# Optimization experiments

Measured on AMD Instinct MI355X. Metric: run time of the kernel, lower is better.

Reference implementation:

```python
import jax, jax.numpy as jnp
import numpy as np

D_MODEL = 512
N_HEADS = 8
POI_N, POI_F = 1683, 24


def _linear_params(k, fan_in, fan_out):
    kw, kb = jax.random.split(k)
    bound = 1.0 / np.sqrt(fan_in)
    w = jax.random.uniform(kw, (fan_in, fan_out), jnp.float32, -bound, bound)
    b = jax.random.uniform(kb, (fan_out,), jnp.float32, -bound, bound)
    return w, b


def setup_inputs() -> dict:
    key = jax.random.key(0)
    ks = jax.random.split(key, 7)
    B, L, D = 8, 8192, D_MODEL
    x = jax.random.normal(ks[0], (B, L, D), jnp.float32)
    poi_data = jax.random.normal(ks[1], (POI_N, POI_F), jnp.float32)
    wq1, bq1 = _linear_params(ks[2], POI_F, 1)
    wq2, bq2 = _linear_params(ks[3], POI_N, D)
    wk, bk = _linear_params(ks[4], D, D)
    wv, bv = _linear_params(ks[5], D, D)
    wo, bo = _linear_params(ks[6], D, D)
    return dict(x=x, poi_data=poi_data, wq1=wq1, bq1=bq1, wq2=wq2, bq2=bq2,
                wk=wk, bk=bk, wv=wv, bv=bv, wo=wo, bo=bo)


def reference(x, poi_data, wq1, bq1, wq2, bq2, wk, bk, wv, bv, wo, bo):
    B, L, D = x.shape
    H = N_HEADS
    d = D // H
    # key / value projections: [B, L, H, d]
    k = (x @ wk + bk).reshape(B, L, H, d)
    v = (x @ wv + bv).reshape(B, L, H, d)
    # query: Linear(24,1) over poi features, squeeze, Linear(1683, d_model)
    q = (poi_data @ wq1 + bq1)[:, 0]          # [1683]
    q = (q @ wq2 + bq2).reshape(H, d)         # [H, d] -- shared across B and L
    scale = 1.0 / jnp.sqrt(jnp.asarray(d, x.dtype))
    # Original computes scores [B,H,L,L] where every row l is identical
    # (query is broadcast over L). Mathematically equivalent collapsed form:
    scores = jnp.einsum('he,bshe->bhs', q, k)  # [B, H, L]
    A = jax.nn.softmax(scale * scores, axis=-1)
    V = jnp.einsum('bhs,bshd->bhd', A, v).reshape(B, H * d)  # [B, D]
    out = jnp.broadcast_to(V[:, None, :], (B, L, H * d))      # same row for all L
    return out @ wo + bo
```

## Files before the change

kernel.cpp:

```cpp
#include <hip/hip_runtime.h>
#include <math.h>

#define L_SEQ 8192
#define B_N   8

typedef float f4v __attribute__((ext_vector_type(4)));

#define QRAW_OFF   0
#define QF_OFF     2048
#define QKV_OFF    2560
#define CK_OFF     6656
#define V_OFF      6720
#define ROW_OFF    10816
#define DPART_OFF  15360
#define YPART_OFF  32768

__global__ void k01_init(float* ws, const float* __restrict__ poi,
                         const float* __restrict__ wq1, const float* __restrict__ bq1,
                         const float* __restrict__ bv, const float* __restrict__ bo,
                         const float* __restrict__ bq2) {
    int gid = blockIdx.x * 256 + threadIdx.x;
    if (gid < 1683) {
        float a = bq1[0];
#pragma unroll
        for (int j = 0; j < 24; ++j) a += poi[gid * 24 + j] * wq1[j];
        ws[QRAW_OFF + gid] = a;
    } else if (gid >= 2048 && gid < 6144) {
        int i = gid - 2048;
        ws[V_OFF + i] = bv[i & 511];
    } else if (gid >= 6144 && gid < 10240) {
        int i = gid - 6144;
        ws[ROW_OFF + i] = bo[i & 511];
    } else if (gid >= 10240 && gid < 10752) {
        ws[QF_OFF + (gid - 10240)] = bq2[gid - 10240];
    }
}

__global__ __launch_bounds__(512) void k2_qf(const float* __restrict__ wq2, float* ws) {
    __shared__ float qr[32];
    int k = blockIdx.x, t = threadIdx.x;
    int i0 = k * 32;
    int cnt = 1683 - i0; if (cnt > 32) cnt = 32;
    if (t < cnt) qr[t] = ws[QRAW_OFF + i0 + t];
    __syncthreads();
    float a = 0.f;
    for (int ii = 0; ii < cnt; ++ii) a += qr[ii] * wq2[(size_t)(i0 + ii) * 512 + t];
    atomicAdd(ws + QF_OFF + t, a);
}

__global__ void k3_qkvec(const float* __restrict__ wk, const float* __restrict__ bk, float* ws) {
    __shared__ float qf[512];
    int t = threadIdx.x;
    for (int t2 = t; t2 < 512; t2 += 256) qf[t2] = ws[QF_OFF + t2];
    __syncthreads();
    int idx = blockIdx.x * 256 + t;
    int h = idx >> 9, c = idx & 511;
    float a = 0.f;
#pragma unroll 8
    for (int e = 0; e < 64; ++e) a += qf[h * 64 + e] * wk[(size_t)c * 512 + h * 64 + e];
    ws[QKV_OFF + idx] = 0.125f * a;
    if (idx < 8) {
        float bsum = 0.f;
        for (int e = 0; e < 64; ++e) bsum += qf[idx * 64 + e] * bk[idx * 64 + e];
        ws[CK_OFF + idx] = 0.125f * bsum;
    }
}

__global__ __launch_bounds__(256, 2) void kF(const float* __restrict__ x, float* __restrict__ ws) {
    int t = threadIdx.x;
    int lane = t & 63, w = t >> 6;
    int b = blockIdx.x >> 6, slot = blockIdx.x & 63;
    int wslot = slot * 4 + w;

    float4 qa[8], qb[8];
    const float4* qk4 = (const float4*)(ws + QKV_OFF);
#pragma unroll
    for (int h = 0; h < 8; ++h) {
        qa[h] = qk4[h * 128 + lane * 2];
        qb[h] = qk4[h * 128 + lane * 2 + 1];
    }
    float ck[8];
#pragma unroll
    for (int h = 0; h < 8; ++h) ck[h] = ws[CK_OFF + h];

    float num[8][8] = {{0.f}};
    float den[8] = {0.f};

    const float4* xp = (const float4*)(x + (size_t)b * L_SEQ * 512);
    float4 cxa = xp[(size_t)wslot * 128 + lane * 2];
    float4 cxb = xp[(size_t)wslot * 128 + lane * 2 + 1];

    for (int r = wslot; r < L_SEQ; r += 256) {
        int rn = r + 256;
        float4 nxa = cxa, nxb = cxb;
        if (rn < L_SEQ) {
            nxa = xp[(size_t)rn * 128 + lane * 2];
            nxb = xp[(size_t)rn * 128 + lane * 2 + 1];
        }
        float p[8];
#pragma unroll
        for (int h = 0; h < 8; ++h)
            p[h] = cxa.x * qa[h].x + cxa.y * qa[h].y + cxa.z * qa[h].z + cxa.w * qa[h].w
                 + cxb.x * qb[h].x + cxb.y * qb[h].y + cxb.z * qb[h].z + cxb.w * qb[h].w;
#pragma unroll
        for (int m = 32; m >= 1; m >>= 1) {
#pragma unroll
            for (int h = 0; h < 8; ++h) p[h] += __shfl_xor(p[h], m, 64);
        }
#pragma unroll
        for (int h = 0; h < 8; ++h) {
            float wg = __expf(p[h] + ck[h]);
            den[h] += wg;
            num[h][0] += wg * cxa.x; num[h][1] += wg * cxa.y;
            num[h][2] += wg * cxa.z; num[h][3] += wg * cxa.w;
            num[h][4] += wg * cxb.x; num[h][5] += wg * cxb.y;
            num[h][6] += wg * cxb.z; num[h][7] += wg * cxb.w;
        }
        cxa = nxa; cxb = nxb;
    }

    __shared__ float num_s[4096];
    __shared__ float den_s[8];
    for (int wi = 0; wi < 4; ++wi) {
        if (w == wi) {
#pragma unroll
            for (int h = 0; h < 8; ++h) {
                int base = h * 512 + lane * 8;
                if (wi == 0) {
#pragma unroll
                    for (int j = 0; j < 8; ++j) num_s[base + j] = num[h][j];
                    if (lane == 0) den_s[h] = den[h];
                } else {
#pragma unroll
                    for (int j = 0; j < 8; ++j) num_s[base + j] += num[h][j];
                    if (lane == 0) den_s[h] += den[h];
                }
            }
        }
        __syncthreads();
    }
    float4* yp4 = (float4*)(ws + YPART_OFF + (size_t)blockIdx.x * 4096);
    const float4* ns4 = (const float4*)num_s;
#pragma unroll
    for (int k = 0; k < 4; ++k) yp4[k * 256 + t] = ns4[k * 256 + t];
    if (t < 8) ws[DPART_OFF + blockIdx.x * 8 + t] = den_s[t];
}

__global__ __launch_bounds__(512) void kV(const float* __restrict__ wv, float* ws) {
    __shared__ float red[512];
    __shared__ float yn_s[512];
    __shared__ float dinv[8];
    int b = blockIdx.x >> 3, cc = blockIdx.x & 7;
    int c0 = cc * 64;
    int t = threadIdx.x;
    red[t] = ws[DPART_OFF + (size_t)(b * 64 + (t >> 3)) * 8 + (t & 7)];
    __syncthreads();
#pragma unroll
    for (int off = 256; off >= 8; off >>= 1) {
        if (t < off) red[t] += red[t + off];
        __syncthreads();
    }
    if (t < 8) dinv[t] = 1.f / red[t];
    int h = t >> 6, cl = t & 63;
    float s = 0.f;
    const float* yp = ws + YPART_OFF + (size_t)(b * 64) * 4096 + h * 512 + c0 + cl;
#pragma unroll 8
    for (int sl = 0; sl < 64; ++sl) s += yp[(size_t)sl * 4096];
    __syncthreads();
    yn_s[t] = s * dinv[h];
    __syncthreads();
    int o = t, ho = o >> 6;
    const float* yh = yn_s + ho * 64;
    float acc = 0.f;
#pragma unroll 8
    for (int ci = 0; ci < 64; ++ci) acc += yh[ci] * wv[(size_t)(c0 + ci) * 512 + o];
    atomicAdd(ws + V_OFF + b * 512 + o, acc);
}

__global__ __launch_bounds__(512) void kRow(const float* __restrict__ wo, float* ws) {
    __shared__ float V_s[64];
    int b = blockIdx.x >> 3, oc = blockIdx.x & 7;
    int o0 = oc * 64;
    int t = threadIdx.x;
    if (t < 64) V_s[t] = ws[V_OFF + b * 512 + o0 + t];
    __syncthreads();
    float acc = 0.f;
#pragma unroll 8
    for (int oi = 0; oi < 64; ++oi) acc += V_s[oi] * wo[(size_t)(o0 + oi) * 512 + t];
    atomicAdd(ws + ROW_OFF + b * 512 + t, acc);
}

__global__ __launch_bounds__(256) void k9_out(const float* __restrict__ ws, float* __restrict__ out) {
    const f4v* row4 = (const f4v*)(ws + ROW_OFF);
    f4v* out4 = (f4v*)out;
    size_t stride = (size_t)gridDim.x * blockDim.x;
    for (size_t g = (size_t)blockIdx.x * blockDim.x + threadIdx.x; g < 8388608ull; g += stride) {
        int b = (int)(g >> 20);
        int q = (int)(g & 127);
        f4v v = row4[b * 128 + q];
        __builtin_nontemporal_store(v, &out4[g]);
    }
}

extern "C" void kernel_launch(void* const* d_in, const int* in_sizes, int n_in,
                              void* d_out, int out_size, void* d_ws, size_t ws_size,
                              hipStream_t stream) {
    const float* x   = (const float*)d_in[0];
    const float* poi = (const float*)d_in[1];
    const float* wq1 = (const float*)d_in[2];
    const float* bq1 = (const float*)d_in[3];
    const float* wq2 = (const float*)d_in[4];
    const float* bq2 = (const float*)d_in[5];
    const float* wk  = (const float*)d_in[6];
    const float* bk  = (const float*)d_in[7];
    const float* wv  = (const float*)d_in[8];
    const float* bv  = (const float*)d_in[9];
    const float* wo  = (const float*)d_in[10];
    const float* bo  = (const float*)d_in[11];
    float* ws  = (float*)d_ws;
    float* out = (float*)d_out;

    k01_init<<<42, 256, 0, stream>>>(ws, poi, wq1, bq1, bv, bo, bq2);
    k2_qf<<<53, 512, 0, stream>>>(wq2, ws);
    k3_qkvec<<<16, 256, 0, stream>>>(wk, bk, ws);
    kF<<<512, 256, 0, stream>>>(x, ws);
    kV<<<64, 512, 0, stream>>>(wv, ws);
    kRow<<<64, 512, 0, stream>>>(wo, ws);
    k9_out<<<2048, 256, 0, stream>>>(ws, out);
}
```

Measured before the change: 103.3 us.

## Fuse init into query kernels, drop bk term, widen main pass to 768 blocks

New measurement: 118.4 us. 14.6% more time.

```diff
diff --git a/kernel.cpp b/kernel.cpp
--- a/kernel.cpp
+++ b/kernel.cpp
@@ -6,70 +6,63 @@
 
 typedef float f4v __attribute__((ext_vector_type(4)));
 
-#define QRAW_OFF   0
-#define QF_OFF     2048
-#define QKV_OFF    2560
-#define CK_OFF     6656
-#define V_OFF      6720
-#define ROW_OFF    10816
-#define DPART_OFF  15360
-#define YPART_OFF  32768
-
-__global__ void k01_init(float* ws, const float* __restrict__ poi,
-                         const float* __restrict__ wq1, const float* __restrict__ bq1,
-                         const float* __restrict__ bv, const float* __restrict__ bo,
-                         const float* __restrict__ bq2) {
-    int gid = blockIdx.x * 256 + threadIdx.x;
-    if (gid < 1683) {
-        float a = bq1[0];
-#pragma unroll
-        for (int j = 0; j < 24; ++j) a += poi[gid * 24 + j] * wq1[j];
-        ws[QRAW_OFF + gid] = a;
-    } else if (gid >= 2048 && gid < 6144) {
-        int i = gid - 2048;
-        ws[V_OFF + i] = bv[i & 511];
-    } else if (gid >= 6144 && gid < 10240) {
-        int i = gid - 6144;
-        ws[ROW_OFF + i] = bo[i & 511];
-    } else if (gid >= 10240 && gid < 10752) {
-        ws[QF_OFF + (gid - 10240)] = bq2[gid - 10240];
-    }
-}
-
-__global__ __launch_bounds__(512) void k2_qf(const float* __restrict__ wq2, float* ws) {
+#define QKV_OFF    0
+#define V_OFF      4096
+#define ROW_OFF    8192
+#define QFP_OFF    12288
+#define DPART_OFF  40960
+#define YPART_OFF  65536
+
+__global__ __launch_bounds__(512) void k2_qf(const float* __restrict__ poi,
+                                             const float* __restrict__ wq1,
+                                             const float* __restrict__ bq1,
+                                             const float* __restrict__ wq2, float* ws) {
     __shared__ float qr[32];
     int k = blockIdx.x, t = threadIdx.x;
     int i0 = k * 32;
     int cnt = 1683 - i0; if (cnt > 32) cnt = 32;
-    if (t < cnt) qr[t] = ws[QRAW_OFF + i0 + t];
+    if (t < cnt) {
+        float a = bq1[0];
+#pragma unroll
+        for (int j = 0; j < 24; ++j) a += poi[(i0 + t) * 24 + j] * wq1[j];
+        qr[t] = a;
+    }
     __syncthreads();
     float a = 0.f;
     for (int ii = 0; ii < cnt; ++ii) a += qr[ii] * wq2[(size_t)(i0 + ii) * 512 + t];
-    atomicAdd(ws + QF_OFF + t, a);
-}
-
-__global__ void k3_qkvec(const float* __restrict__ wk, const float* __restrict__ bk, float* ws) {
+    ws[QFP_OFF + k * 512 + t] = a;
+}
+
+__global__ void k3_qkvec(const float* __restrict__ wk, const float* __restrict__ bq2,
+                         const float* __restrict__ bv, const float* __restrict__ bo, float* ws) {
     __shared__ float qf[512];
-    int t = threadIdx.x;
-    for (int t2 = t; t2 < 512; t2 += 256) qf[t2] = ws[QF_OFF + t2];
-    __syncthreads();
-    int idx = blockIdx.x * 256 + t;
+    int t = threadIdx.x, bid = blockIdx.x;
+    for (int o = t; o < 512; o += 256) {
+        float s = bq2[o];
+        for (int k = 0; k < 53; ++k) s += ws[QFP_OFF + k * 512 + o];
+        qf[o] = s;
+    }
+    __syncthreads();
+    int idx = bid * 256 + t;
     int h = idx >> 9, c = idx & 511;
     float a = 0.f;
 #pragma unroll 8
     for (int e = 0; e < 64; ++e) a += qf[h * 64 + e] * wk[(size_t)c * 512 + h * 64 + e];
     ws[QKV_OFF + idx] = 0.125f * a;
-    if (idx < 8) {
-        float bsum = 0.f;
-        for (int e = 0; e < 64; ++e) bsum += qf[idx * 64 + e] * bk[idx * 64 + e];
-        ws[CK_OFF + idx] = 0.125f * bsum;
-    }
-}
-
-__global__ __launch_bounds__(256, 2) void kF(const float* __restrict__ x, float* __restrict__ ws) {
+    if (bid < 8) {
+        ws[V_OFF + bid * 512 + t]       = bv[t];
+        ws[V_OFF + bid * 512 + 256 + t] = bv[256 + t];
+    } else {
+        int b = bid - 8;
+        ws[ROW_OFF + b * 512 + t]       = bo[t];
+        ws[ROW_OFF + b * 512 + 256 + t] = bo[256 + t];
+    }
+}
+
+__global__ __launch_bounds__(256, 3) void kF(const float* __restrict__ x, float* __restrict__ ws) {
     int t = threadIdx.x;
     int lane = t & 63, w = t >> 6;
-    int b = blockIdx.x >> 6, slot = blockIdx.x & 63;
+    int b = blockIdx.x / 96, slot = blockIdx.x % 96;
     int wslot = slot * 4 + w;
 
     float4 qa[8], qb[8];
@@ -79,9 +72,6 @@
         qa[h] = qk4[h * 128 + lane * 2];
         qb[h] = qk4[h * 128 + lane * 2 + 1];
     }
-    float ck[8];
-#pragma unroll
-    for (int h = 0; h < 8; ++h) ck[h] = ws[CK_OFF + h];
 
     float num[8][8] = {{0.f}};
     float den[8] = {0.f};
@@ -90,8 +80,8 @@
     float4 cxa = xp[(size_t)wslot * 128 + lane * 2];
     float4 cxb = xp[(size_t)wslot * 128 + lane * 2 + 1];
 
-    for (int r = wslot; r < L_SEQ; r += 256) {
-        int rn = r + 256;
+    for (int r = wslot; r < L_SEQ; r += 384) {
+        int rn = r + 384;
         float4 nxa = cxa, nxb = cxb;
         if (rn < L_SEQ) {
             nxa = xp[(size_t)rn * 128 + lane * 2];
@@ -109,7 +99,7 @@
         }
 #pragma unroll
         for (int h = 0; h < 8; ++h) {
-            float wg = __expf(p[h] + ck[h]);
+            float wg = __expf(p[h]);
             den[h] += wg;
             num[h][0] += wg * cxa.x; num[h][1] += wg * cxa.y;
             num[h][2] += wg * cxa.z; num[h][3] += wg * cxa.w;
@@ -153,7 +143,13 @@
     int b = blockIdx.x >> 3, cc = blockIdx.x & 7;
     int c0 = cc * 64;
     int t = threadIdx.x;
-    red[t] = ws[DPART_OFF + (size_t)(b * 64 + (t >> 3)) * 8 + (t & 7)];
+    {
+        int s0 = t >> 3, hh = t & 7;
+        const float* dp = ws + DPART_OFF + (size_t)(b * 96) * 8 + hh;
+        float v = dp[(size_t)s0 * 8];
+        if (s0 < 32) v += dp[(size_t)(64 + s0) * 8];
+        red[t] = v;
+    }
     __syncthreads();
 #pragma unroll
     for (int off = 256; off >= 8; off >>= 1) {
@@ -163,9 +159,9 @@
     if (t < 8) dinv[t] = 1.f / red[t];
     int h = t >> 6, cl = t & 63;
     float s = 0.f;
-    const float* yp = ws + YPART_OFF + (size_t)(b * 64) * 4096 + h * 512 + c0 + cl;
-#pragma unroll 8
-    for (int sl = 0; sl < 64; ++sl) s += yp[(size_t)sl * 4096];
+    const float* yp = ws + YPART_OFF + (size_t)(b * 96) * 4096 + h * 512 + c0 + cl;
+#pragma unroll 8
+    for (int sl = 0; sl < 96; ++sl) s += yp[(size_t)sl * 4096];
     __syncthreads();
     yn_s[t] = s * dinv[h];
     __syncthreads();
@@ -219,11 +215,11 @@
     const float* bo  = (const float*)d_in[11];
     float* ws  = (float*)d_ws;
     float* out = (float*)d_out;
-
-    k01_init<<<42, 256, 0, stream>>>(ws, poi, wq1, bq1, bv, bo, bq2);
-    k2_qf<<<53, 512, 0, stream>>>(wq2, ws);
-    k3_qkvec<<<16, 256, 0, stream>>>(wk, bk, ws);
-    kF<<<512, 256, 0, stream>>>(x, ws);
+    (void)bk;
+
+    k2_qf<<<53, 512, 0, stream>>>(poi, wq1, bq1, wq2, ws);
+    k3_qkvec<<<16, 256, 0, stream>>>(wk, bq2, bv, bo, ws);
+    kF<<<768, 256, 0, stream>>>(x, ws);
     kV<<<64, 512, 0, stream>>>(wv, ws);
     kRow<<<64, 512, 0, stream>>>(wo, ws);
     k9_out<<<2048, 256, 0, stream>>>(ws, out);
```
